# Optimization experiments

Hardware: AMD Instinct MI355X
Metric: run time of the kernel (lower is better)

The kernel has to match this reference:

```python
import jax, jax.numpy as jnp
import numpy as np

N_NODES = 100000
N_EDGES = 1600000
D = 128


def setup_inputs() -> dict:
    key = jax.random.key(0)
    k0, k1, k2, k3 = jax.random.split(key, 4)
    x = jax.random.normal(k0, (N_NODES, D), dtype=jnp.float32)
    edge_index = jax.random.randint(k1, (2, N_EDGES), 0, N_NODES, dtype=jnp.int32)
    # Glorot-ish init for GCNConv weights; zero bias (PyG default)
    W1 = jax.random.normal(k2, (D, D), dtype=jnp.float32) / np.sqrt(D).astype(np.float32)
    b1 = jnp.zeros((D,), dtype=jnp.float32)
    W2 = jax.random.normal(k3, (D, D), dtype=jnp.float32) / np.sqrt(D).astype(np.float32)
    b2 = jnp.zeros((D,), dtype=jnp.float32)
    return {"x": x, "edge_index": edge_index, "W1": W1, "b1": b1, "W2": W2, "b2": b2}


def _gcn_layer(x, src, dst, norm, W, b, n_nodes):
    # PyG GCNConv: linear transform first, then normalized aggregation over A+I.
    h = x @ W                                    # [N, D_out]
    coef = norm[src] * norm[dst]                 # [E] symmetric normalization
    msgs = h[src] * coef[:, None]                # [E, D_out] gathered edge messages
    agg = jax.ops.segment_sum(msgs, dst, num_segments=n_nodes)
    agg = agg + h * (norm * norm)[:, None]       # self-loop contribution deg^{-1} * h
    return agg + b


def reference(x, edge_index, W1, b1, W2, b2):
    n_nodes = x.shape[0]
    src, dst = edge_index[0], edge_index[1]
    # degree of A + I (self-loops added), computed on destination nodes
    deg = jax.ops.segment_sum(jnp.ones(src.shape[0], dtype=x.dtype), dst,
                              num_segments=n_nodes) + 1.0
    norm = jax.lax.rsqrt(deg)                    # deg^{-1/2}
    # Layer 1: GCNConv -> ReLU (dropout is identity in eval mode)
    h = jax.nn.relu(_gcn_layer(x, src, dst, norm, W1, b1, n_nodes))
    # Layer 2
    h = jax.nn.relu(_gcn_layer(h, src, dst, norm, W2, b2, n_nodes))
    return h
```

## Files before the change

### kernel.cpp

```cpp
#include <hip/hip_runtime.h>

#define D 128
#define EG 4096

typedef _Float16 h8 __attribute__((ext_vector_type(8)));
typedef float f4 __attribute__((ext_vector_type(4)));


__global__ __launch_bounds__(256) void hist_k(const int* __restrict__ dst,
                                              int* __restrict__ counts,
                                              int E, int NB, int G) {
  __shared__ int hist[512];
  int g = blockIdx.x, t = threadIdx.x;
  for (int b = t; b < NB; b += 256) hist[b] = 0;
  __syncthreads();
  int e0 = g * EG;
#pragma unroll
  for (int it = 0; it < EG / 256; ++it) {
    int e = e0 + it * 256 + t;
    if (e < E) atomicAdd(&hist[dst[e] >> 8], 1);
  }
  __syncthreads();
  for (int b = t; b < NB; b += 256) counts[b * G + g] = hist[b];
}

__global__ __launch_bounds__(256) void bsum_k(const int* __restrict__ in,
                                              int* __restrict__ bsum, int M) {
  __shared__ int s[256];
  int t = threadIdx.x, i = blockIdx.x * 256 + t;
  s[t] = (i < M) ? in[i] : 0;
  __syncthreads();
  for (int off = 128; off > 0; off >>= 1) {
    if (t < off) s[t] += s[t + off];
    __syncthreads();
  }
  if (t == 0) bsum[blockIdx.x] = s[0];
}

__global__ __launch_bounds__(1024) void bscan_k(int* bsum, int nb) {
  __shared__ int s[1024];
  int t = threadIdx.x;
  s[t] = (t < nb) ? bsum[t] : 0;
  __syncthreads();
  for (int off = 1; off < 1024; off <<= 1) {
    int v = (t >= off) ? s[t - off] : 0;
    __syncthreads();
    s[t] += v;
    __syncthreads();
  }
  if (t < nb) bsum[t] = s[t];
}

__global__ __launch_bounds__(256) void scanfin_k(const int* __restrict__ in,
                                                 const int* __restrict__ bsum_incl,
                                                 int* __restrict__ outx, int M) {
  __shared__ int s[256];
  int b = blockIdx.x, t = threadIdx.x, i = b * 256 + t;
  int v0 = (i < M) ? in[i] : 0;
  s[t] = v0;
  __syncthreads();
  for (int off = 1; off < 256; off <<= 1) {
    int v = (t >= off) ? s[t - off] : 0;
    __syncthreads();
    s[t] += v;
    __syncthreads();
  }
  int base = (b > 0) ? bsum_incl[b - 1] : 0;
  if (i < M) outx[i] = base + s[t] - v0;
}

__global__ __launch_bounds__(256) void scatter_k(const int* __restrict__ src,
                                                 const int* __restrict__ dst,
                                                 const int* __restrict__ cscan,
                                                 unsigned* __restrict__ tmp,
                                                 int E, int NB, int G) {
  __shared__ int hist[512];
  __shared__ int base[512];
  int g = blockIdx.x, t = threadIdx.x;
  for (int b = t; b < NB; b += 256) {
    hist[b] = 0;
    base[b] = cscan[b * G + g];
  }
  __syncthreads();
  int e0 = g * EG;
#pragma unroll
  for (int it = 0; it < EG / 256; ++it) {
    int e = e0 + it * 256 + t;
    if (e < E) {
      int d = dst[e];
      int b = d >> 8;
      int r = atomicAdd(&hist[b], 1);
      tmp[base[b] + r] = ((unsigned)(d & 255) << 20) | (unsigned)src[e];
    }
  }
}

__global__ __launch_bounds__(256) void bucket_k(const unsigned* __restrict__ tmp,
                                                const int* __restrict__ cscan,
                                                float* __restrict__ nrm,
                                                int* __restrict__ row_start,
                                                int* __restrict__ esrc,
                                                int N, int E, int NB, int G) {
  __shared__ int cnt[256];
  __shared__ int sc[256];
  __shared__ int cur[256];
  int b = blockIdx.x, t = threadIdx.x;
  int seg0 = cscan[b * G];
  int seg1 = (b == NB - 1) ? E : cscan[(b + 1) * G];
  cnt[t] = 0;
  __syncthreads();
  for (int i = seg0 + t; i < seg1; i += 256)
    atomicAdd(&cnt[tmp[i] >> 20], 1);
  __syncthreads();
  int v0 = cnt[t];
  sc[t] = v0;
  __syncthreads();
  for (int off = 1; off < 256; off <<= 1) {
    int v = (t >= off) ? sc[t - off] : 0;
    __syncthreads();
    sc[t] += v;
    __syncthreads();
  }
  int ex = sc[t] - v0;
  cur[t] = ex;
  int node = b * 256 + t;
  if (node < N) {
    row_start[node] = seg0 + ex;
    nrm[node] = rsqrtf((float)v0 + 1.0f);
  }
  if (b == 0 && t == 0) row_start[N] = E;
  __syncthreads();
  for (int i = seg0 + t; i < seg1; i += 256) {
    unsigned p = tmp[i];
    int r = atomicAdd(&cur[p >> 20], 1);
    esrc[seg0 + r] = (int)(p & 0xFFFFF);
  }
}

__global__ __launch_bounds__(256) void wtrans_k(const float* __restrict__ W,
                                                _Float16* __restrict__ WT) {
  int idx = blockIdx.x * 256 + threadIdx.x;
  int k = idx >> 7, col = idx & 127;
  WT[col * D + k] = (_Float16)W[idx];
}

template <bool FP32IN>
__global__ __launch_bounds__(256) void gemm_k(const void* __restrict__ Xv,
                                              const _Float16* __restrict__ WT,
                                              const float* __restrict__ nrm,
                                              _Float16* __restrict__ Hh, int N) {
  __shared__ _Float16 Wl[D * 136];
  int tid = threadIdx.x;
#pragma unroll
  for (int it = 0; it < 8; ++it) {
    int idx = it * 256 + tid;
    int col = idx >> 4, kseg = idx & 15;
    *(h8*)&Wl[col * 136 + kseg * 8] = *(const h8*)&WT[col * D + kseg * 8];
  }
  __syncthreads();
  int wave = tid >> 6, lane = tid & 63;
  int lr = lane & 15, lk = lane >> 4;
#pragma unroll
  for (int tt = 0; tt < 2; ++tt) {
    int tile = blockIdx.x * 8 + wave * 2 + tt;
    int row0 = tile * 16;
    if (row0 >= N) break;
    int row = row0 + lr;
    int rowc = row < N ? row : N - 1;
    h8 a[4];
    if constexpr (FP32IN) {
      const float* X = (const float*)Xv;
#pragma unroll
      for (int ks = 0; ks < 4; ++ks) {
        f4 p = *(const f4*)&X[(size_t)rowc * D + ks * 32 + lk * 8];
        f4 q = *(const f4*)&X[(size_t)rowc * D + ks * 32 + lk * 8 + 4];
        h8 t;
        t[0] = (_Float16)p[0]; t[1] = (_Float16)p[1];
        t[2] = (_Float16)p[2]; t[3] = (_Float16)p[3];
        t[4] = (_Float16)q[0]; t[5] = (_Float16)q[1];
        t[6] = (_Float16)q[2]; t[7] = (_Float16)q[3];
        a[ks] = t;
      }
    } else {
      const _Float16* X = (const _Float16*)Xv;
#pragma unroll
      for (int ks = 0; ks < 4; ++ks)
        a[ks] = *(const h8*)&X[(size_t)rowc * D + ks * 32 + lk * 8];
    }
    f4 acc[8];
#pragma unroll
    for (int ct = 0; ct < 8; ++ct) acc[ct] = (f4){0.f, 0.f, 0.f, 0.f};
#pragma unroll
    for (int ct = 0; ct < 8; ++ct) {
#pragma unroll
      for (int ks = 0; ks < 4; ++ks) {
        h8 b = *(const h8*)&Wl[(ct * 16 + lr) * 136 + ks * 32 + lk * 8];
        acc[ct] = __builtin_amdgcn_mfma_f32_16x16x32_f16(a[ks], b, acc[ct], 0, 0, 0);
      }
    }
#pragma unroll
    for (int r = 0; r < 4; ++r) {
      int ro = row0 + lk * 4 + r;
      if (ro < N) {
        float sc = nrm[ro];
#pragma unroll
        for (int ct = 0; ct < 8; ++ct)
          Hh[(size_t)ro * D + ct * 16 + lr] = (_Float16)(acc[ct][r] * sc);
      }
    }
  }
}

#define ACC8(A, v)                                                        \
  {                                                                       \
    A[0] += (float)v[0]; A[1] += (float)v[1]; A[2] += (float)v[2];        \
    A[3] += (float)v[3]; A[4] += (float)v[4]; A[5] += (float)v[5];        \
    A[6] += (float)v[6]; A[7] += (float)v[7];                             \
  }

template <bool F16OUT>
__global__ __launch_bounds__(256) void agg_k(const _Float16* __restrict__ Hh,
                                             const float* __restrict__ nrm,
                                             const int* __restrict__ row_start,
                                             const int* __restrict__ esrc,
                                             const float* __restrict__ bias,
                                             void* __restrict__ outv, int N) {
  int wave = threadIdx.x >> 6, lane = threadIdx.x & 63;
  int n = blockIdx.x * 4 + wave;
  if (n >= N) return;
  int grp = lane >> 4, sub = lane & 15;
  int d0 = sub * 8;
  int i0 = row_start[n], end = row_start[n + 1];
  float a0[8] = {}, a1[8] = {}, a2[8] = {}, a3[8] = {};
  for (int i = i0; i < end; i += 16) {
    int e0 = i + grp, e1 = i + 4 + grp, e2 = i + 8 + grp, e3 = i + 12 + grp;
    if (e3 < end) {
      int s0 = esrc[e0], s1 = esrc[e1], s2 = esrc[e2], s3 = esrc[e3];
      h8 v0 = *(const h8*)&Hh[(size_t)s0 * D + d0];
      h8 v1 = *(const h8*)&Hh[(size_t)s1 * D + d0];
      h8 v2 = *(const h8*)&Hh[(size_t)s2 * D + d0];
      h8 v3 = *(const h8*)&Hh[(size_t)s3 * D + d0];
      ACC8(a0, v0); ACC8(a1, v1); ACC8(a2, v2); ACC8(a3, v3);
    } else {
      if (e0 < end) {
        int s0 = esrc[e0];
        h8 v0 = *(const h8*)&Hh[(size_t)s0 * D + d0];
        ACC8(a0, v0);
      }
      if (e1 < end) {
        int s1 = esrc[e1];
        h8 v1 = *(const h8*)&Hh[(size_t)s1 * D + d0];
        ACC8(a1, v1);
      }
      if (e2 < end) {
        int s2 = esrc[e2];
        h8 v2 = *(const h8*)&Hh[(size_t)s2 * D + d0];
        ACC8(a2, v2);
      }
    }
  }
  float r[8];
#pragma unroll
  for (int j = 0; j < 8; ++j) r[j] = (a0[j] + a1[j]) + (a2[j] + a3[j]);
#pragma unroll
  for (int j = 0; j < 8; ++j) r[j] += __shfl_xor(r[j], 16);
#pragma unroll
  for (int j = 0; j < 8; ++j) r[j] += __shfl_xor(r[j], 32);
  if (grp == 0) {
    h8 hv = *(const h8*)&Hh[(size_t)n * D + d0];
    float nn = nrm[n];
    f4 bl = *(const f4*)&bias[d0];
    f4 bh = *(const f4*)&bias[d0 + 4];
    float o[8];
#pragma unroll
    for (int j = 0; j < 8; ++j) {
      float bj = (j < 4) ? bl[j] : bh[j - 4];
      o[j] = fmaxf((r[j] + (float)hv[j]) * nn + bj, 0.f);
    }
    if constexpr (F16OUT) {
      _Float16* out = (_Float16*)outv;
      h8 ov;
#pragma unroll
      for (int j = 0; j < 8; ++j) ov[j] = (_Float16)o[j];
      *(h8*)&out[(size_t)n * D + d0] = ov;
    } else {
      float* out = (float*)outv;
      f4 lo = {o[0], o[1], o[2], o[3]};
      f4 hi = {o[4], o[5], o[6], o[7]};
      *(f4*)&out[(size_t)n * D + d0] = lo;
      *(f4*)&out[(size_t)n * D + d0 + 4] = hi;
    }
  }
}


extern "C" void kernel_launch(void* const* d_in, const int* in_sizes, int n_in,
                              void* d_out, int out_size, void* d_ws, size_t ws_size,
                              hipStream_t stream) {
  const float* x  = (const float*)d_in[0];
  const int*   ei = (const int*)d_in[1];
  const float* W1 = (const float*)d_in[2];
  const float* b1 = (const float*)d_in[3];
  const float* W2 = (const float*)d_in[4];
  const float* b2 = (const float*)d_in[5];
  float* out = (float*)d_out;

  int N = in_sizes[0] / D;
  int E = in_sizes[1] / 2;
  const int* srcp = ei;
  const int* dstp = ei + E;

  int NB = (N + 255) / 256;
  int G  = (E + EG - 1) / EG;
  int M  = NB * G;
  int nbM = (M + 255) / 256;

  char* ws = (char*)d_ws;
  size_t off = 0;
  auto alloc = [&](size_t bytes) -> char* {
    char* p = ws + off;
    off = (off + bytes + 511) & ~(size_t)511;
    return p;
  };
  _Float16* Hh   = (_Float16*)alloc((size_t)N * D * 2);
  _Float16* O1h  = (_Float16*)alloc((size_t)N * D * 2);
  float* normv     = (float*)alloc((size_t)N * 4);
  int*   row_start = (int*)alloc((size_t)(N + 1) * 4);
  int*   counts    = (int*)alloc((size_t)M * 4);
  int*   cscan     = (int*)alloc((size_t)M * 4);
  unsigned* tmp    = (unsigned*)alloc((size_t)E * 4);
  int*   esrc      = (int*)alloc((size_t)E * 4);
  int*   bsum      = (int*)alloc(4096);
  _Float16* WT1    = (_Float16*)alloc((size_t)D * D * 2);
  _Float16* WT2    = (_Float16*)alloc((size_t)D * D * 2);

  int tiles = (N + 15) / 16;
  int nbGemm = (tiles + 7) / 8;
  int nbAgg = (N + 3) / 4;

  wtrans_k<<<64, 256, 0, stream>>>(W1, WT1);
  wtrans_k<<<64, 256, 0, stream>>>(W2, WT2);

  hist_k<<<G, 256, 0, stream>>>(dstp, counts, E, NB, G);
  bsum_k<<<nbM, 256, 0, stream>>>(counts, bsum, M);
  bscan_k<<<1, 1024, 0, stream>>>(bsum, nbM);
  scanfin_k<<<nbM, 256, 0, stream>>>(counts, bsum, cscan, M);
  scatter_k<<<G, 256, 0, stream>>>(srcp, dstp, cscan, tmp, E, NB, G);
  bucket_k<<<NB, 256, 0, stream>>>(tmp, cscan, normv, row_start, esrc, N, E, NB, G);

  gemm_k<true><<<nbGemm, 256, 0, stream>>>(x, WT1, normv, Hh, N);
  agg_k<true><<<nbAgg, 256, 0, stream>>>(Hh, normv, row_start, esrc, b1, O1h, N);
  gemm_k<false><<<nbGemm, 256, 0, stream>>>(O1h, WT2, normv, Hh, N);
  agg_k<false><<<nbAgg, 256, 0, stream>>>(Hh, normv, row_start, esrc, b2, out, N);
}
```

Baseline: 232.4 us.

## Pad CSR rows to multiples of 8 with a zero dummy row and branchless fdot2 aggregation

```diff
diff --git a/kernel.cpp b/kernel.cpp
--- a/kernel.cpp
+++ b/kernel.cpp
@@ -2,9 +2,12 @@
 
 #define D 128
 #define EG 4096
+#define PADW 8
 
 typedef _Float16 h8 __attribute__((ext_vector_type(8)));
+typedef _Float16 h2 __attribute__((ext_vector_type(2)));
 typedef float f4 __attribute__((ext_vector_type(4)));
+typedef unsigned u4 __attribute__((ext_vector_type(4)));
 
 
 __global__ __launch_bounds__(256) void hist_k(const int* __restrict__ dst,
@@ -98,8 +101,8 @@
 __global__ __launch_bounds__(256) void bucket_k(const unsigned* __restrict__ tmp,
                                                 const int* __restrict__ cscan,
                                                 float* __restrict__ nrm,
-                                                int* __restrict__ row_start,
-                                                int* __restrict__ esrc,
+                                                int2* __restrict__ rs2,
+                                                int* __restrict__ eoff,
                                                 int N, int E, int NB, int G) {
   __shared__ int cnt[256];
   __shared__ int sc[256];
@@ -107,13 +110,15 @@
   int b = blockIdx.x, t = threadIdx.x;
   int seg0 = cscan[b * G];
   int seg1 = (b == NB - 1) ? E : cscan[(b + 1) * G];
+  int pbase = seg0 + b * 256 * (PADW - 1);
   cnt[t] = 0;
   __syncthreads();
   for (int i = seg0 + t; i < seg1; i += 256)
     atomicAdd(&cnt[tmp[i] >> 20], 1);
   __syncthreads();
   int v0 = cnt[t];
-  sc[t] = v0;
+  int pd = (v0 + PADW - 1) & ~(PADW - 1);
+  sc[t] = pd;
   __syncthreads();
   for (int off = 1; off < 256; off <<= 1) {
     int v = (t >= off) ? sc[t - off] : 0;
@@ -121,20 +126,26 @@
     sc[t] += v;
     __syncthreads();
   }
-  int ex = sc[t] - v0;
-  cur[t] = ex;
+  int ex = sc[t] - pd;
+  cur[t] = pbase + ex;
   int node = b * 256 + t;
   if (node < N) {
-    row_start[node] = seg0 + ex;
+    rs2[node] = make_int2(pbase + ex, pbase + ex + pd);
     nrm[node] = rsqrtf((float)v0 + 1.0f);
   }
-  if (b == 0 && t == 0) row_start[N] = E;
+  int dummy = N * 256;
+  for (int k = v0; k < pd; ++k) eoff[pbase + ex + k] = dummy;
   __syncthreads();
   for (int i = seg0 + t; i < seg1; i += 256) {
     unsigned p = tmp[i];
     int r = atomicAdd(&cur[p >> 20], 1);
-    esrc[seg0 + r] = (int)(p & 0xFFFFF);
-  }
+    eoff[r] = (int)((p & 0xFFFFF) << 8);
+  }
+}
+
+__global__ void zero_k(_Float16* __restrict__ Hh, int N) {
+  int t = threadIdx.x;
+  if (t < 128) Hh[(size_t)N * D + t] = (_Float16)0.f;
 }
 
 __global__ __launch_bounds__(256) void wtrans_k(const float* __restrict__ W,
@@ -211,62 +222,44 @@
   }
 }
 
-#define ACC8(A, v)                                                        \
-  {                                                                       \
-    A[0] += (float)v[0]; A[1] += (float)v[1]; A[2] += (float)v[2];        \
-    A[3] += (float)v[3]; A[4] += (float)v[4]; A[5] += (float)v[5];        \
-    A[6] += (float)v[6]; A[7] += (float)v[7];                             \
-  }
-
 template <bool F16OUT>
 __global__ __launch_bounds__(256) void agg_k(const _Float16* __restrict__ Hh,
                                              const float* __restrict__ nrm,
-                                             const int* __restrict__ row_start,
-                                             const int* __restrict__ esrc,
+                                             const int2* __restrict__ rs2,
+                                             const int* __restrict__ eoff,
                                              const float* __restrict__ bias,
                                              void* __restrict__ outv, int N) {
   int wave = threadIdx.x >> 6, lane = threadIdx.x & 63;
   int n = blockIdx.x * 4 + wave;
   if (n >= N) return;
   int grp = lane >> 4, sub = lane & 15;
-  int d0 = sub * 8;
-  int i0 = row_start[n], end = row_start[n + 1];
-  float a0[8] = {}, a1[8] = {}, a2[8] = {}, a3[8] = {};
-  for (int i = i0; i < end; i += 16) {
-    int e0 = i + grp, e1 = i + 4 + grp, e2 = i + 8 + grp, e3 = i + 12 + grp;
-    if (e3 < end) {
-      int s0 = esrc[e0], s1 = esrc[e1], s2 = esrc[e2], s3 = esrc[e3];
-      h8 v0 = *(const h8*)&Hh[(size_t)s0 * D + d0];
-      h8 v1 = *(const h8*)&Hh[(size_t)s1 * D + d0];
-      h8 v2 = *(const h8*)&Hh[(size_t)s2 * D + d0];
-      h8 v3 = *(const h8*)&Hh[(size_t)s3 * D + d0];
-      ACC8(a0, v0); ACC8(a1, v1); ACC8(a2, v2); ACC8(a3, v3);
-    } else {
-      if (e0 < end) {
-        int s0 = esrc[e0];
-        h8 v0 = *(const h8*)&Hh[(size_t)s0 * D + d0];
-        ACC8(a0, v0);
-      }
-      if (e1 < end) {
-        int s1 = esrc[e1];
-        h8 v1 = *(const h8*)&Hh[(size_t)s1 * D + d0];
-        ACC8(a1, v1);
-      }
-      if (e2 < end) {
-        int s2 = esrc[e2];
-        h8 v2 = *(const h8*)&Hh[(size_t)s2 * D + d0];
-        ACC8(a2, v2);
-      }
-    }
-  }
-  float r[8];
-#pragma unroll
-  for (int j = 0; j < 8; ++j) r[j] = (a0[j] + a1[j]) + (a2[j] + a3[j]);
-#pragma unroll
-  for (int j = 0; j < 8; ++j) r[j] += __shfl_xor(r[j], 16);
-#pragma unroll
-  for (int j = 0; j < 8; ++j) r[j] += __shfl_xor(r[j], 32);
+  unsigned soff = (unsigned)sub * 16u;
+  int2 se = rs2[n];
+  const char* base = (const char*)Hh;
+  const h2 ones = {(_Float16)1.f, (_Float16)1.f};
+  float acc[8] = {};
+  for (int i = se.x; i < se.y; i += PADW) {
+    int e0 = i + grp * 2;
+    unsigned o0 = (unsigned)eoff[e0] + soff;
+    unsigned o1 = (unsigned)eoff[e0 + 1] + soff;
+    u4 v0 = *(const u4*)(base + o0);
+    u4 v1 = *(const u4*)(base + o1);
+#pragma unroll
+    for (int k = 0; k < 4; ++k) {
+      unsigned lo = __builtin_amdgcn_perm(v1[k], v0[k], 0x05040100u);
+      unsigned hi = __builtin_amdgcn_perm(v1[k], v0[k], 0x07060302u);
+      acc[2 * k] = __builtin_amdgcn_fdot2(__builtin_bit_cast(h2, lo), ones,
+                                          acc[2 * k], false);
+      acc[2 * k + 1] = __builtin_amdgcn_fdot2(__builtin_bit_cast(h2, hi), ones,
+                                              acc[2 * k + 1], false);
+    }
+  }
+#pragma unroll
+  for (int j = 0; j < 8; ++j) acc[j] += __shfl_xor(acc[j], 16);
+#pragma unroll
+  for (int j = 0; j < 8; ++j) acc[j] += __shfl_xor(acc[j], 32);
   if (grp == 0) {
+    int d0 = sub * 8;
     h8 hv = *(const h8*)&Hh[(size_t)n * D + d0];
     float nn = nrm[n];
     f4 bl = *(const f4*)&bias[d0];
@@ -275,7 +268,7 @@
 #pragma unroll
     for (int j = 0; j < 8; ++j) {
       float bj = (j < 4) ? bl[j] : bh[j - 4];
-      o[j] = fmaxf((r[j] + (float)hv[j]) * nn + bj, 0.f);
+      o[j] = fmaxf((acc[j] + (float)hv[j]) * nn + bj, 0.f);
     }
     if constexpr (F16OUT) {
       _Float16* out = (_Float16*)outv;
@@ -322,14 +315,14 @@
     off = (off + bytes + 511) & ~(size_t)511;
     return p;
   };
-  _Float16* Hh   = (_Float16*)alloc((size_t)N * D * 2);
+  _Float16* Hh   = (_Float16*)alloc((size_t)(N + 1) * D * 2);
   _Float16* O1h  = (_Float16*)alloc((size_t)N * D * 2);
   float* normv     = (float*)alloc((size_t)N * 4);
-  int*   row_start = (int*)alloc((size_t)(N + 1) * 4);
+  int2*  rs2       = (int2*)alloc((size_t)N * 8);
   int*   counts    = (int*)alloc((size_t)M * 4);
   int*   cscan     = (int*)alloc((size_t)M * 4);
   unsigned* tmp    = (unsigned*)alloc((size_t)E * 4);
-  int*   esrc      = (int*)alloc((size_t)E * 4);
+  int*   eoff      = (int*)alloc((size_t)(E + NB * 256 * (PADW - 1)) * 4);
   int*   bsum      = (int*)alloc(4096);
   _Float16* WT1    = (_Float16*)alloc((size_t)D * D * 2);
   _Float16* WT2    = (_Float16*)alloc((size_t)D * D * 2);
@@ -340,16 +333,17 @@
 
   wtrans_k<<<64, 256, 0, stream>>>(W1, WT1);
   wtrans_k<<<64, 256, 0, stream>>>(W2, WT2);
+  zero_k<<<1, 128, 0, stream>>>(Hh, N);
 
   hist_k<<<G, 256, 0, stream>>>(dstp, counts, E, NB, G);
   bsum_k<<<nbM, 256, 0, stream>>>(counts, bsum, M);
   bscan_k<<<1, 1024, 0, stream>>>(bsum, nbM);
   scanfin_k<<<nbM, 256, 0, stream>>>(counts, bsum, cscan, M);
   scatter_k<<<G, 256, 0, stream>>>(srcp, dstp, cscan, tmp, E, NB, G);
-  bucket_k<<<NB, 256, 0, stream>>>(tmp, cscan, normv, row_start, esrc, N, E, NB, G);
+  bucket_k<<<NB, 256, 0, stream>>>(tmp, cscan, normv, rs2, eoff, N, E, NB, G);
 
   gemm_k<true><<<nbGemm, 256, 0, stream>>>(x, WT1, normv, Hh, N);
-  agg_k<true><<<nbAgg, 256, 0, stream>>>(Hh, normv, row_start, esrc, b1, O1h, N);
+  agg_k<true><<<nbAgg, 256, 0, stream>>>(Hh, normv, rs2, eoff, b1, O1h, N);
   gemm_k<false><<<nbGemm, 256, 0, stream>>>(O1h, WT2, normv, Hh, N);
-  agg_k<false><<<nbAgg, 256, 0, stream>>>(Hh, normv, row_start, esrc, b2, out, N);
-}
+  agg_k<false><<<nbAgg, 256, 0, stream>>>(Hh, normv, rs2, eoff, b2, out, N);
+}
```

Measured after the change: 220.9 us. 1.05x faster.
